# Performance work log

Measured on AMD Instinct MI355X. Metric: run time of the kernel, lower is better.

## Reference

```python
import jax, jax.numpy as jnp
import numpy as np

N_NODES = 100000
N_EDGES = 1600000
IN_FEATS = 128
N_HIDDEN = 64
N_HEADS = 4
N_CLASSES = 16


def setup_inputs() -> dict:
    key = jax.random.key(0)
    ks = jax.random.split(key, 16)
    h = jax.random.normal(ks[0], (N_NODES, IN_FEATS), dtype=jnp.float32)
    src = jax.random.randint(ks[1], (N_EDGES,), 0, N_NODES, dtype=jnp.int32)
    dst = jax.random.randint(ks[2], (N_EDGES,), 0, N_NODES, dtype=jnp.int32)
    def xavier(k, shape, fan_in, fan_out):
        gain = jnp.sqrt(2.0)  # calculate_gain('relu')
        std = gain * jnp.sqrt(2.0 / (fan_in + fan_out))
        return (std * jax.random.normal(k, shape)).astype(jnp.float32)
    # layer 1: per-head W [H, in, out], A [H, 2*out]
    W1 = xavier(ks[3], (N_HEADS, IN_FEATS, N_HIDDEN), IN_FEATS, N_HIDDEN)
    b1 = jnp.zeros((N_HEADS, N_HIDDEN), jnp.float32)
    a1 = xavier(ks[4], (N_HEADS, 2 * N_HIDDEN), 2 * N_HIDDEN, 1)
    ab1 = jnp.zeros((N_HEADS,), jnp.float32)
    # layer 2: input is concat of heads = N_HEADS*N_HIDDEN, output n_classes, heads averaged
    d2 = N_HEADS * N_HIDDEN
    W2 = xavier(ks[5], (N_HEADS, d2, N_CLASSES), d2, N_CLASSES)
    b2 = jnp.zeros((N_HEADS, N_CLASSES), jnp.float32)
    a2 = xavier(ks[6], (N_HEADS, 2 * N_CLASSES), 2 * N_CLASSES, 1)
    ab2 = jnp.zeros((N_HEADS,), jnp.float32)
    fc_w = xavier(ks[7], (N_CLASSES, N_CLASSES), N_CLASSES, N_CLASSES)
    fc_b = jnp.zeros((N_CLASSES,), jnp.float32)
    return dict(h=h, src=src, dst=dst, W1=W1, b1=b1, a1=a1, ab1=ab1,
                W2=W2, b2=b2, a2=a2, ab2=ab2, fc_w=fc_w, fc_b=fc_b)


def gat_layer(h, src, dst, W, b, a, ab, n_nodes):
    # h: [N, F]; W: [H, F, O]; a: [H, 2O]
    O = W.shape[-1]
    Wh = jnp.einsum('nf,hfo->nho', h, W) + b          # [N, H, O]
    Wh_src = Wh[src]                                   # [E, H, O] (messages Wh_j)
    Wh_dst = Wh[dst]                                   # [E, H, O] (Wh_i)
    # e_ij = LeakyReLU(A([Wh_i, Wh_j]), 0.2)
    e = (jnp.einsum('eho,ho->eh', Wh_dst, a[:, :O])
         + jnp.einsum('eho,ho->eh', Wh_src, a[:, O:]) + ab)  # [E, H]
    e = jax.nn.leaky_relu(e, 0.2)
    # segment softmax over incoming edges of each dst node
    m = jax.ops.segment_max(e, dst, num_segments=n_nodes)     # [N, H] (-inf for empty)
    ex = jnp.exp(e - m[dst])
    denom = jax.ops.segment_sum(ex, dst, num_segments=n_nodes)
    alpha = ex / denom[dst]                                    # [E, H]
    # weighted neighbor aggregation (zero for zero-in-degree nodes, as DGL)
    out = jax.ops.segment_sum(alpha[:, :, None] * Wh_src, dst, num_segments=n_nodes)
    return out  # [N, H, O]


def reference(h, src, dst, W1, b1, a1, ab1, W2, b2, a2, ab2, fc_w, fc_b):
    n = h.shape[0]
    # layer 1 (heads concatenated) + ELU; dropout = identity (eval mode)
    h1 = gat_layer(h, src, dst, W1, b1, a1, ab1, n)            # [N, H, n_hidden]
    h1 = jax.nn.elu(h1.reshape(n, -1))                         # [N, H*n_hidden]
    # layer 2 (heads averaged) + softmax over features
    h2 = gat_layer(h1, src, dst, W2, b2, a2, ab2, n).mean(axis=1)  # [N, n_classes]
    h2 = jax.nn.softmax(h2, axis=1)
    # readout: mean over nodes, then fc
    hg = h2.mean(axis=0)                                        # [n_classes]
    return hg @ fc_w.T + fc_b
```

## Files before the change

kernel.cpp:

```cpp
#include <hip/hip_runtime.h>
#include <math.h>

#define N_NODES  100000
#define N_EDGES  1600000
#define IN_F     128
#define HID      64
#define HEADS    4
#define NCLS     16
#define D1       (HEADS*HID)
#define D2       (HEADS*NCLS)

#define SCAN_CHUNK 1024
#define SCAN_NB    ((N_NODES + SCAN_CHUNK - 1) / SCAN_CHUNK)
#define N_NODES_PAD (SCAN_NB * SCAN_CHUNK)
#define RB1 128
#define AGG_BLOCKS 2048
#define AGG_WAVES  (AGG_BLOCKS * 4)

typedef __attribute__((ext_vector_type(8))) short bf16x8_t;
typedef __attribute__((ext_vector_type(4))) float f32x4_t;
typedef __attribute__((ext_vector_type(2))) float f32x2_t;

__device__ __forceinline__ unsigned bf16rne(float x) {
  unsigned u = __float_as_uint(x);
  return (u + 0x7fffu + ((u >> 16) & 1u)) >> 16;
}
__device__ __forceinline__ unsigned packbf2(float lo, float hi) {
  return bf16rne(lo) | (bf16rne(hi) << 16);
}

__global__ __launch_bounds__(256)
void k_zero4(int4* __restrict__ p, int n4) {
  int i = blockIdx.x * blockDim.x + threadIdx.x;
  if (i < n4) p[i] = make_int4(0, 0, 0, 0);
}

__global__ __launch_bounds__(256)
void k_count(const int* __restrict__ dst, int* __restrict__ cursorPad,
             int* __restrict__ rank) {
  int i = blockIdx.x * blockDim.x + threadIdx.x;
  if (i < N_EDGES) {
    int d = dst[i];
    rank[i] = atomicAdd(&cursorPad[d << 4], 1);
  }
}

__global__ __launch_bounds__(256)
void k_compact(const int* __restrict__ cursorPad, int* __restrict__ counts) {
  int i = blockIdx.x * blockDim.x + threadIdx.x;
  if (i < N_NODES_PAD) counts[i] = (i < N_NODES) ? cursorPad[i << 4] : 0;
}

__global__ __launch_bounds__(256)
void k_scanA(const int* __restrict__ counts, int* __restrict__ btot) {
  __shared__ int red[256];
  int t = threadIdx.x;
  const int4* cp = (const int4*)(counts + blockIdx.x * SCAN_CHUNK);
  int4 v = cp[t];
  red[t] = v.x + v.y + v.z + v.w;
  __syncthreads();
  for (int s = 128; s; s >>= 1) {
    if (t < s) red[t] += red[t + s];
    __syncthreads();
  }
  if (t == 0) btot[blockIdx.x] = red[0];
}

__global__ __launch_bounds__(128)
void k_scanB(const int* __restrict__ btot, int* __restrict__ bbase,
             int* __restrict__ offs) {
  __shared__ int part[128];
  int t = threadIdx.x;
  part[t] = (t < SCAN_NB) ? btot[t] : 0;
  __syncthreads();
  for (int o = 1; o < 128; o <<= 1) {
    int v = (t >= o) ? part[t - o] : 0;
    __syncthreads();
    part[t] += v;
    __syncthreads();
  }
  if (t < SCAN_NB) bbase[t] = (t == 0) ? 0 : part[t - 1];
  if (t == 0) offs[N_NODES] = N_EDGES;
}

__global__ __launch_bounds__(256)
void k_scanC(const int* __restrict__ counts, const int* __restrict__ bbase,
             int* __restrict__ offs) {
  __shared__ int part[256];
  int t = threadIdx.x;
  int gbase = blockIdx.x * SCAN_CHUNK;
  const int4* cp = (const int4*)(counts + gbase);
  int4 v = cp[t];
  int tot = v.x + v.y + v.z + v.w;
  part[t] = tot;
  __syncthreads();
  for (int o = 1; o < 256; o <<= 1) {
    int q = (t >= o) ? part[t - o] : 0;
    __syncthreads();
    part[t] += q;
    __syncthreads();
  }
  int run = bbase[blockIdx.x] + part[t] - tot;
  int i0 = gbase + t * 4;
  int o0 = run;
  int o1 = o0 + v.x;
  int o2 = o1 + v.y;
  int o3 = o2 + v.z;
  if (i0 + 0 < N_NODES) offs[i0 + 0] = o0;
  if (i0 + 1 < N_NODES) offs[i0 + 1] = o1;
  if (i0 + 2 < N_NODES) offs[i0 + 2] = o2;
  if (i0 + 3 < N_NODES) offs[i0 + 3] = o3;
}

__global__ __launch_bounds__(256)
void k_scatter(const int* __restrict__ src, const int* __restrict__ dst,
               const int* __restrict__ rank, const int* __restrict__ offs,
               int* __restrict__ csrsrc) {
  int i = blockIdx.x * blockDim.x + threadIdx.x;
  if (i < N_EDGES) {
    csrsrc[offs[dst[i]] + rank[i]] = src[i];
  }
}

__global__ __launch_bounds__(256)
void k_prepw(const float* __restrict__ W1, const float* __restrict__ W2,
             unsigned* __restrict__ W1t32, unsigned* __restrict__ W2t32) {
  int t = threadIdx.x;
  if (blockIdx.x == 0) {
    int c = t;
    const float* wp = W1 + ((c >> 6) << 13) + (c & 63);
    unsigned* op = W1t32 + c * 64;
    for (int fp = 0; fp < 64; ++fp) {
      float lo = wp[(2 * fp) << 6];
      float hi = wp[(2 * fp + 1) << 6];
      op[fp] = packbf2(lo, hi);
    }
  } else {
    int c = t & 63, fq = t >> 6;
    const float* wp = W2 + ((c >> 4) << 12) + (c & 15);
    unsigned* op = W2t32 + c * 128 + fq * 32;
    for (int fp = 0; fp < 32; ++fp) {
      int f0 = fq * 64 + 2 * fp;
      op[fp] = packbf2(wp[f0 << 4], wp[(f0 + 1) << 4]);
    }
  }
}

__global__ __launch_bounds__(256)
void k_gemm1(const float* __restrict__ h, const unsigned short* __restrict__ W1t,
             const float* __restrict__ bias, const float* __restrict__ a1,
             unsigned char* __restrict__ Wh8,
             float* __restrict__ sD, float* __restrict__ sS) {
  __shared__ float aLds[512];
  int t = threadIdx.x;
  aLds[t] = a1[t];
  aLds[t + 256] = a1[t + 256];
  __syncthreads();

  int wv = t >> 6;
  int lane = t & 63;
  int m = lane & 15;
  int q8 = (lane >> 4) * 8;
  int node = blockIdx.x * 64 + wv * 16 + m;
  int nclamp = node < N_NODES ? node : N_NODES - 1;

  f32x4_t acc[16] = {};
  const float* hp0 = h + (size_t)nclamp * IN_F + q8;
  #pragma unroll
  for (int ks = 0; ks < 4; ++ks) {
    int kk = ks * 32;
    float4 f0 = *(const float4*)(hp0 + kk);
    float4 f1 = *(const float4*)(hp0 + kk + 4);
    bf16x8_t bf;
    bf[0] = (short)bf16rne(f0.x); bf[1] = (short)bf16rne(f0.y);
    bf[2] = (short)bf16rne(f0.z); bf[3] = (short)bf16rne(f0.w);
    bf[4] = (short)bf16rne(f1.x); bf[5] = (short)bf16rne(f1.y);
    bf[6] = (short)bf16rne(f1.z); bf[7] = (short)bf16rne(f1.w);
    #pragma unroll
    for (int ct = 0; ct < 16; ++ct) {
      bf16x8_t af = *(const bf16x8_t*)(W1t + (ct * 16 + m) * IN_F + kk + q8);
      acc[ct] = __builtin_amdgcn_mfma_f32_16x16x32_bf16(af, bf, acc[ct], 0, 0, 0);
    }
  }
  if (node < N_NODES) {
    unsigned char* op = Wh8 + (size_t)node * D1;
    int quad4 = (lane >> 4) * 4;
    float pd[4] = {}, ps[4] = {};
    #pragma unroll
    for (int ct = 0; ct < 16; ++ct) {
      int c0 = ct * 16 + quad4;
      float4 bb = *(const float4*)(bias + c0);
      float v0 = acc[ct][0] + bb.x, v1 = acc[ct][1] + bb.y;
      float v2 = acc[ct][2] + bb.z, v3 = acc[ct][3] + bb.w;
      int hh = ct >> 2;
      const float* aD = &aLds[hh * 128 + (c0 & 63)];
      pd[hh] += v0 * aD[0] + v1 * aD[1] + v2 * aD[2] + v3 * aD[3];
      ps[hh] += v0 * aD[64] + v1 * aD[65] + v2 * aD[66] + v3 * aD[67];
      int pk = __builtin_amdgcn_cvt_pk_fp8_f32(v0, v1, 0, false);
      pk = __builtin_amdgcn_cvt_pk_fp8_f32(v2, v3, pk, true);
      *(unsigned*)(op + c0) = (unsigned)pk;
    }
    #pragma unroll
    for (int hh = 0; hh < 4; ++hh) {
      pd[hh] += __shfl_xor(pd[hh], 16); pd[hh] += __shfl_xor(pd[hh], 32);
      ps[hh] += __shfl_xor(ps[hh], 16); ps[hh] += __shfl_xor(ps[hh], 32);
    }
    if (lane < 16) {
      ((float4*)sD)[node] = make_float4(pd[0], pd[1], pd[2], pd[3]);
      ((float4*)sS)[node] = make_float4(ps[0], ps[1], ps[2], ps[3]);
    }
  }
}

__global__ __launch_bounds__(256)
void k_gemm2(const unsigned short* __restrict__ h1b, const unsigned short* __restrict__ W2t,
             const float* __restrict__ bias, const float* __restrict__ a2,
             unsigned short* __restrict__ Whb2,
             float* __restrict__ sD, float* __restrict__ sS) {
  __shared__ float aLds[128];
  int t = threadIdx.x;
  if (t < 128) aLds[t] = a2[t];
  __syncthreads();

  int wv = t >> 6;
  int lane = t & 63;
  int m = lane & 15;
  int q8 = (lane >> 4) * 8;
  int node = blockIdx.x * 64 + wv * 16 + m;
  int nclamp = node < N_NODES ? node : N_NODES - 1;

  f32x4_t acc[4] = {};
  const unsigned short* hp0 = h1b + (size_t)nclamp * D1 + q8;
  #pragma unroll
  for (int ks = 0; ks < 8; ++ks) {
    int kk = ks * 32;
    bf16x8_t bf = *(const bf16x8_t*)(hp0 + kk);
    #pragma unroll
    for (int ct = 0; ct < 4; ++ct) {
      bf16x8_t af = *(const bf16x8_t*)(W2t + (ct * 16 + m) * D1 + kk + q8);
      acc[ct] = __builtin_amdgcn_mfma_f32_16x16x32_bf16(af, bf, acc[ct], 0, 0, 0);
    }
  }
  if (node < N_NODES) {
    unsigned short* op = Whb2 + (size_t)node * D2;
    int quad4 = (lane >> 4) * 4;
    float pd[4] = {}, ps[4] = {};
    #pragma unroll
    for (int ct = 0; ct < 4; ++ct) {
      int c0 = ct * 16 + quad4;
      float4 bb = *(const float4*)(bias + c0);
      float v0 = acc[ct][0] + bb.x, v1 = acc[ct][1] + bb.y;
      float v2 = acc[ct][2] + bb.z, v3 = acc[ct][3] + bb.w;
      const float* aD = &aLds[ct * 32 + (c0 & 15)];
      pd[ct] += v0 * aD[0] + v1 * aD[1] + v2 * aD[2] + v3 * aD[3];
      ps[ct] += v0 * aD[16] + v1 * aD[17] + v2 * aD[18] + v3 * aD[19];
      uint2 o;
      o.x = packbf2(v0, v1);
      o.y = packbf2(v2, v3);
      *(uint2*)(op + c0) = o;
    }
    #pragma unroll
    for (int hh = 0; hh < 4; ++hh) {
      pd[hh] += __shfl_xor(pd[hh], 16); pd[hh] += __shfl_xor(pd[hh], 32);
      ps[hh] += __shfl_xor(ps[hh], 16); ps[hh] += __shfl_xor(ps[hh], 32);
    }
    if (lane < 16) {
      ((float4*)sD)[node] = make_float4(pd[0], pd[1], pd[2], pd[3]);
      ((float4*)sS)[node] = make_float4(ps[0], ps[1], ps[2], ps[3]);
    }
  }
}

__device__ __forceinline__ float lrelu(float x) { return x > 0.f ? x : 0.2f * x; }
__device__ __forceinline__ float elu(float x)   { return x > 0.f ? x : expm1f(x); }

__global__ __launch_bounds__(256)
void k_agg1(const int* __restrict__ offs, const int* __restrict__ csrsrc,
            const float* __restrict__ sD, const float* __restrict__ sS,
            const float* __restrict__ ab,
            const unsigned char* __restrict__ Wh8, unsigned short* __restrict__ h1out) {
  __shared__ float exbuf[4][64 * 4];
  __shared__ int   offbuf[4][64];
  int wv = threadIdx.x >> 6;
  int lane = threadIdx.x & 63;
  int g = lane >> 5;
  int l = lane & 31;
  int hh = l >> 3;
  unsigned lb = (unsigned)(l << 3);
  float ab0 = ab[0], ab1 = ab[1], ab2 = ab[2], ab3 = ab[3];
  const float* eb = exbuf[wv];
  const int* ob = offbuf[wv];

  for (int wid = blockIdx.x * 4 + wv; wid < N_NODES; wid += AGG_WAVES) {
    float acc[8] = {};
    float z0 = 0.f, z1 = 0.f, z2 = 0.f, z3 = 0.f;
    int beg = offs[wid], end = offs[wid + 1];
    bool nonempty = end > beg;
    if (nonempty) {
      float4 dv = ((const float4*)sD)[wid];
      float db0 = dv.x + ab0, db1 = dv.y + ab1;
      float db2 = dv.z + ab2, db3 = dv.w + ab3;
      for (int cbeg = beg; cbeg < end; cbeg += 64) {
        int j = cbeg + lane;
        int cnt = end - cbeg; if (cnt > 64) cnt = 64;
        int sid = 0;
        float e0 = 0.f, e1 = 0.f, e2 = 0.f, e3 = 0.f;
        if (j < end) {
          sid = csrsrc[j];
          float4 sv = ((const float4*)sS)[sid];
          e0 = __expf(lrelu(db0 + sv.x));
          e1 = __expf(lrelu(db1 + sv.y));
          e2 = __expf(lrelu(db2 + sv.z));
          e3 = __expf(lrelu(db3 + sv.w));
          z0 += e0; z1 += e1; z2 += e2; z3 += e3;
        }
        offbuf[wv][lane] = sid << 8;
        *(float4*)&exbuf[wv][lane * 4] = make_float4(e0, e1, e2, e3);
        int npairs = (cnt + 1) >> 1;
        int nh = (npairs + 1) >> 1;
        for (int u = 0; u < nh; ++u) {
          int iA = 2 * u + g;
          int iB = iA + 2 * nh;
          float wA = eb[iA * 4 + hh];
          float wB = eb[iB * 4 + hh];
          unsigned vA = (unsigned)ob[iA] + lb;
          unsigned vB = (unsigned)ob[iB] + lb;
          uint2 pA = *(const uint2*)(Wh8 + vA);
          uint2 pB = *(const uint2*)(Wh8 + vB);
          f32x2_t a0 = __builtin_amdgcn_cvt_pk_f32_fp8(pA.x, false);
          f32x2_t a1v = __builtin_amdgcn_cvt_pk_f32_fp8(pA.x, true);
          f32x2_t a2v = __builtin_amdgcn_cvt_pk_f32_fp8(pA.y, false);
          f32x2_t a3 = __builtin_amdgcn_cvt_pk_f32_fp8(pA.y, true);
          acc[0] = fmaf(wA, a0[0], acc[0]);
          acc[1] = fmaf(wA, a0[1], acc[1]);
          acc[2] = fmaf(wA, a1v[0], acc[2]);
          acc[3] = fmaf(wA, a1v[1], acc[3]);
          acc[4] = fmaf(wA, a2v[0], acc[4]);
          acc[5] = fmaf(wA, a2v[1], acc[5]);
          acc[6] = fmaf(wA, a3[0], acc[6]);
          acc[7] = fmaf(wA, a3[1], acc[7]);
          f32x2_t b0 = __builtin_amdgcn_cvt_pk_f32_fp8(pB.x, false);
          f32x2_t b1 = __builtin_amdgcn_cvt_pk_f32_fp8(pB.x, true);
          f32x2_t b2 = __builtin_amdgcn_cvt_pk_f32_fp8(pB.y, false);
          f32x2_t b3 = __builtin_amdgcn_cvt_pk_f32_fp8(pB.y, true);
          acc[0] = fmaf(wB, b0[0], acc[0]);
          acc[1] = fmaf(wB, b0[1], acc[1]);
          acc[2] = fmaf(wB, b1[0], acc[2]);
          acc[3] = fmaf(wB, b1[1], acc[3]);
          acc[4] = fmaf(wB, b2[0], acc[4]);
          acc[5] = fmaf(wB, b2[1], acc[5]);
          acc[6] = fmaf(wB, b3[0], acc[6]);
          acc[7] = fmaf(wB, b3[1], acc[7]);
        }
      }
      #pragma unroll
      for (int o = 32; o; o >>= 1) {
        z0 += __shfl_xor(z0, o);
        z1 += __shfl_xor(z1, o);
        z2 += __shfl_xor(z2, o);
        z3 += __shfl_xor(z3, o);
      }
    }
    #pragma unroll
    for (int i = 0; i < 8; ++i) acc[i] += __shfl_xor(acc[i], 32);
    float z = (hh == 0) ? z0 : (hh == 1) ? z1 : (hh == 2) ? z2 : z3;
    if (!nonempty) z = 1.f;
    float inv = 1.f / z;
    if (g == 0) {
      float e0 = elu(acc[0] * inv), e1 = elu(acc[1] * inv);
      float e2 = elu(acc[2] * inv), e3 = elu(acc[3] * inv);
      float e4 = elu(acc[4] * inv), e5 = elu(acc[5] * inv);
      float e6 = elu(acc[6] * inv), e7 = elu(acc[7] * inv);
      uint4 o;
      o.x = packbf2(e0, e1);
      o.y = packbf2(e2, e3);
      o.z = packbf2(e4, e5);
      o.w = packbf2(e6, e7);
      *(uint4*)(h1out + (size_t)wid * D1 + l * 8) = o;
    }
  }
}

__global__ __launch_bounds__(256)
void k_agg2(const int* __restrict__ offs, const int* __restrict__ csrsrc,
            const float* __restrict__ sD, const float* __restrict__ sS,
            const float* __restrict__ ab,
            const unsigned short* __restrict__ Whb2, float* __restrict__ partials) {
  __shared__ float exbuf[4][64 * 4];
  __shared__ int   offbuf[4][64];
  __shared__ float red[4][16];
  int wv = threadIdx.x >> 6;
  int lane = threadIdx.x & 63;
  int g = lane >> 4;
  int l = lane & 15;
  int hh = l >> 2;
  unsigned lb = (unsigned)(l << 3);
  float ab0 = ab[0], ab1 = ab[1], ab2 = ab[2], ab3 = ab[3];
  const float* eb = exbuf[wv];
  const int* ob = offbuf[wv];
  float smacc[4] = {};

  for (int wid = blockIdx.x * 4 + wv; wid < N_NODES; wid += AGG_WAVES) {
    float acc[4] = {};
    float z0 = 0.f, z1 = 0.f, z2 = 0.f, z3 = 0.f;
    int beg = offs[wid], end = offs[wid + 1];
    bool nonempty = end > beg;
    if (nonempty) {
      float4 dv = ((const float4*)sD)[wid];
      float db0 = dv.x + ab0, db1 = dv.y + ab1;
      float db2 = dv.z + ab2, db3 = dv.w + ab3;
      for (int cbeg = beg; cbeg < end; cbeg += 64) {
        int j = cbeg + lane;
        int cnt = end - cbeg; if (cnt > 64) cnt = 64;
        int sid = 0;
        float e0 = 0.f, e1 = 0.f, e2 = 0.f, e3 = 0.f;
        if (j < end) {
          sid = csrsrc[j];
          float4 sv = ((const float4*)sS)[sid];
          e0 = __expf(lrelu(db0 + sv.x));
          e1 = __expf(lrelu(db1 + sv.y));
          e2 = __expf(lrelu(db2 + sv.z));
          e3 = __expf(lrelu(db3 + sv.w));
          z0 += e0; z1 += e1; z2 += e2; z3 += e3;
        }
        offbuf[wv][lane] = sid << 7;
        *(float4*)&exbuf[wv][lane * 4] = make_float4(e0, e1, e2, e3);
        int ni = (cnt + 3) >> 2;
        int nh2 = (ni + 1) >> 1;
        for (int it = 0; it < nh2; ++it) {
          int qA = 4 * it + g;
          int qB = qA + 4 * nh2;
          float wA = eb[qA * 4 + hh];
          float wB = eb[qB * 4 + hh];
          unsigned vA = (unsigned)ob[qA] + lb;
          unsigned vB = (unsigned)ob[qB] + lb;
          uint2 pA = *(const uint2*)((const unsigned char*)Whb2 + vA);
          uint2 pB = *(const uint2*)((const unsigned char*)Whb2 + vB);
          acc[0] = fmaf(wA, __uint_as_float(pA.x << 16), acc[0]);
          acc[1] = fmaf(wA, __uint_as_float(pA.x & 0xffff0000u), acc[1]);
          acc[2] = fmaf(wA, __uint_as_float(pA.y << 16), acc[2]);
          acc[3] = fmaf(wA, __uint_as_float(pA.y & 0xffff0000u), acc[3]);
          acc[0] = fmaf(wB, __uint_as_float(pB.x << 16), acc[0]);
          acc[1] = fmaf(wB, __uint_as_float(pB.x & 0xffff0000u), acc[1]);
          acc[2] = fmaf(wB, __uint_as_float(pB.y << 16), acc[2]);
          acc[3] = fmaf(wB, __uint_as_float(pB.y & 0xffff0000u), acc[3]);
        }
      }
      #pragma unroll
      for (int s = 32; s; s >>= 1) {
        z0 += __shfl_xor(z0, s);
        z1 += __shfl_xor(z1, s);
        z2 += __shfl_xor(z2, s);
        z3 += __shfl_xor(z3, s);
      }
    }
    #pragma unroll
    for (int i = 0; i < 4; ++i) {
      acc[i] += __shfl_xor(acc[i], 16);
      acc[i] += __shfl_xor(acc[i], 32);
    }
    float z = (hh == 0) ? z0 : (hh == 1) ? z1 : (hh == 2) ? z2 : z3;
    if (!nonempty) z = 1.f;
    float inv = 1.f / z;
    float val[4];
    #pragma unroll
    for (int i = 0; i < 4; ++i) val[i] = acc[i] * inv;
    #pragma unroll
    for (int i = 0; i < 4; ++i) {
      val[i] += __shfl_xor(val[i], 4);
      val[i] += __shfl_xor(val[i], 8);
      val[i] *= 0.25f;
    }
    float mx = fmaxf(fmaxf(val[0], val[1]), fmaxf(val[2], val[3]));
    mx = fmaxf(mx, __shfl_xor(mx, 1));
    mx = fmaxf(mx, __shfl_xor(mx, 2));
    float e[4];
    float ssum = 0.f;
    #pragma unroll
    for (int i = 0; i < 4; ++i) { e[i] = __expf(val[i] - mx); ssum += e[i]; }
    ssum += __shfl_xor(ssum, 1);
    ssum += __shfl_xor(ssum, 2);
    float rinv = 1.f / ssum;
    #pragma unroll
    for (int i = 0; i < 4; ++i) smacc[i] += e[i] * rinv;
  }

  if (g == 0 && l < 4) {
    #pragma unroll
    for (int i = 0; i < 4; ++i) red[wv][l * 4 + i] = smacc[i];
  }
  __syncthreads();
  if (threadIdx.x < 16) {
    partials[(size_t)blockIdx.x * 16 + threadIdx.x] =
        red[0][threadIdx.x] + red[1][threadIdx.x] +
        red[2][threadIdx.x] + red[3][threadIdx.x];
  }
}

__global__ __launch_bounds__(256)
void k_reduce1(const float* __restrict__ partials, int nrows,
               float* __restrict__ out) {
  __shared__ float red[16][17];
  int t = threadIdx.x;
  int c = t & 15, rl = t >> 4;
  int per = (nrows + RB1 - 1) / RB1;
  int rbeg = blockIdx.x * per;
  int rend = rbeg + per; if (rend > nrows) rend = nrows;
  float s = 0.f;
  for (int r = rbeg + rl; r < rend; r += 16) s += partials[(size_t)r * 16 + c];
  red[rl][c] = s;
  __syncthreads();
  for (int st = 8; st; st >>= 1) {
    if (rl < st) red[rl][c] += red[rl + st][c];
    __syncthreads();
  }
  if (t < 16) out[(size_t)blockIdx.x * 16 + t] = red[0][t];
}

__global__ __launch_bounds__(256)
void k_final(const float* __restrict__ partials,
             const float* __restrict__ fcw, const float* __restrict__ fcb,
             float* __restrict__ out) {
  __shared__ float red[16][17];
  __shared__ float hg[16];
  int t = threadIdx.x;
  int c = t & 15, rl = t >> 4;
  float s = 0.f;
  for (int r = rl; r < RB1; r += 16) s += partials[(size_t)r * 16 + c];
  red[rl][c] = s;
  __syncthreads();
  for (int st = 8; st; st >>= 1) {
    if (rl < st) red[rl][c] += red[rl + st][c];
    __syncthreads();
  }
  if (t < 16) hg[t] = red[0][t] * (1.0f / N_NODES);
  __syncthreads();
  if (t < 16) {
    float acc = fcb[t];
    #pragma unroll
    for (int k = 0; k < 16; ++k) acc += hg[k] * fcw[t * 16 + k];
    out[t] = acc;
  }
}

extern "C" void kernel_launch(void* const* d_in, const int* in_sizes, int n_in,
                              void* d_out, int out_size, void* d_ws, size_t ws_size,
                              hipStream_t stream) {
  const float* h   = (const float*)d_in[0];
  const int*   src = (const int*)  d_in[1];
  const int*   dst = (const int*)  d_in[2];
  const float* W1  = (const float*)d_in[3];
  const float* b1  = (const float*)d_in[4];
  const float* a1  = (const float*)d_in[5];
  const float* ab1 = (const float*)d_in[6];
  const float* W2  = (const float*)d_in[7];
  const float* b2  = (const float*)d_in[8];
  const float* a2  = (const float*)d_in[9];
  const float* ab2 = (const float*)d_in[10];
  const float* fcw = (const float*)d_in[11];
  const float* fcb = (const float*)d_in[12];
  float* out = (float*)d_out;

  char* ws = (char*)d_ws;
  size_t off = 0;
  auto alloc = [&](size_t bytes) -> char* {
    char* p = ws + off;
    off += (bytes + 255) & ~(size_t)255;
    return p;
  };
  unsigned char*  Wh8  = (unsigned char*)alloc((size_t)N_NODES * D1);
  unsigned short* h1b  = (unsigned short*)alloc((size_t)N_NODES * D1 * 2);
  unsigned short* Whb2 = (unsigned short*)alloc((size_t)N_NODES * D2 * 2);
  unsigned short* W1t  = (unsigned short*)alloc((size_t)D1 * IN_F * 2);
  unsigned short* W2t  = (unsigned short*)alloc((size_t)D2 * D1 * 2);
  float* sD1 = (float*)alloc((size_t)N_NODES * 4 * 4);
  float* sS1 = (float*)alloc((size_t)N_NODES * 4 * 4);
  float* sD2 = (float*)alloc((size_t)N_NODES * 4 * 4);
  float* sS2 = (float*)alloc((size_t)N_NODES * 4 * 4);
  int* cursorPad = (int*)alloc((size_t)N_NODES * 16 * 4);
  int* rank   = (int*)alloc((size_t)N_EDGES * 4);
  int* counts = (int*)alloc((size_t)N_NODES_PAD * 4);
  int* offs   = (int*)alloc((size_t)(N_NODES + 1) * 4);
  int* csrsrc = (int*)alloc((size_t)N_EDGES * 4);
  int* btot   = (int*)alloc((size_t)SCAN_NB * 4);
  int* bbase  = (int*)alloc((size_t)SCAN_NB * 4);
  float* partials  = (float*)alloc((size_t)AGG_BLOCKS * 16 * 4);
  float* partials2 = (float*)alloc((size_t)RB1 * 16 * 4);

  k_prepw<<<2, 256, 0, stream>>>(W1, W2, (unsigned*)W1t, (unsigned*)W2t);

  const int n4 = N_NODES * 4;
  k_zero4<<<(n4 + 255) / 256, 256, 0, stream>>>((int4*)cursorPad, n4);
  k_count<<<(N_EDGES + 255) / 256, 256, 0, stream>>>(dst, cursorPad, rank);
  k_compact<<<(N_NODES_PAD + 255) / 256, 256, 0, stream>>>(cursorPad, counts);
  k_scanA<<<SCAN_NB, 256, 0, stream>>>(counts, btot);
  k_scanB<<<1, 128, 0, stream>>>(btot, bbase, offs);
  k_scanC<<<SCAN_NB, 256, 0, stream>>>(counts, bbase, offs);
  k_scatter<<<(N_EDGES + 255) / 256, 256, 0, stream>>>(src, dst, rank, offs, csrsrc);

  const int gemmBlocks = (N_NODES + 63) / 64;

  k_gemm1<<<gemmBlocks, 256, 0, stream>>>(h, W1t, b1, a1, Wh8, sD1, sS1);
  k_agg1<<<AGG_BLOCKS, 256, 0, stream>>>(offs, csrsrc, sD1, sS1, ab1, Wh8, h1b);

  k_gemm2<<<gemmBlocks, 256, 0, stream>>>(h1b, W2t, b2, a2, Whb2, sD2, sS2);
  k_agg2<<<AGG_BLOCKS, 256, 0, stream>>>(offs, csrsrc, sD2, sS2, ab2, Whb2, partials);

  k_reduce1<<<RB1, 256, 0, stream>>>(partials, AGG_BLOCKS, partials2);
  k_final<<<1, 256, 0, stream>>>(partials2, fcw, fcb, out);
}
```

Measured before the change: 480.6 us.

## Fuse CSR-build kernels, vectorize edge passes, use packed FMA in aggregation

Merges weight prep with the cursor zeroing, and the count compaction with the first scan stage. This removes two launches. The edge count and scatter kernels now process four edges per thread with int4 loads. The gemm1 launch moves between count and scan. Both aggregation kernels switch to packed two-wide f32 FMA on vector accumulators to cut VALU instruction count. Risks are extra register shuffling for the vector splits and unchanged atomic contention.

```diff
diff --git a/kernel.cpp b/kernel.cpp
--- a/kernel.cpp
+++ b/kernel.cpp
@@ -16,6 +16,9 @@
 #define RB1 128
 #define AGG_BLOCKS 2048
 #define AGG_WAVES  (AGG_BLOCKS * 4)
+#define GEMM1_BLOCKS ((N_NODES + 63) / 64)
+#define EDGE4_BLOCKS ((N_EDGES / 4 + 255) / 256)
+#define ZERO_BLOCKS  ((N_NODES * 4 + 255) / 256)
 
 typedef __attribute__((ext_vector_type(8))) short bf16x8_t;
 typedef __attribute__((ext_vector_type(4))) float f32x4_t;
@@ -28,36 +31,65 @@
 __device__ __forceinline__ unsigned packbf2(float lo, float hi) {
   return bf16rne(lo) | (bf16rne(hi) << 16);
 }
-
-__global__ __launch_bounds__(256)
-void k_zero4(int4* __restrict__ p, int n4) {
-  int i = blockIdx.x * blockDim.x + threadIdx.x;
-  if (i < n4) p[i] = make_int4(0, 0, 0, 0);
-}
-
-__global__ __launch_bounds__(256)
-void k_count(const int* __restrict__ dst, int* __restrict__ cursorPad,
-             int* __restrict__ rank) {
-  int i = blockIdx.x * blockDim.x + threadIdx.x;
-  if (i < N_EDGES) {
-    int d = dst[i];
-    rank[i] = atomicAdd(&cursorPad[d << 4], 1);
-  }
-}
-
-__global__ __launch_bounds__(256)
-void k_compact(const int* __restrict__ cursorPad, int* __restrict__ counts) {
-  int i = blockIdx.x * blockDim.x + threadIdx.x;
-  if (i < N_NODES_PAD) counts[i] = (i < N_NODES) ? cursorPad[i << 4] : 0;
-}
-
-__global__ __launch_bounds__(256)
-void k_scanA(const int* __restrict__ counts, int* __restrict__ btot) {
+__device__ __forceinline__ f32x2_t pkfma(f32x2_t a, f32x2_t b, f32x2_t c) {
+  return __builtin_elementwise_fma(a, b, c);
+}
+
+__global__ __launch_bounds__(256)
+void k_prep(const float* __restrict__ W1, const float* __restrict__ W2,
+            unsigned* __restrict__ W1t32, unsigned* __restrict__ W2t32,
+            int4* __restrict__ cursorPad4) {
+  int t = threadIdx.x;
+  if (blockIdx.x == 0) {
+    int c = t;
+    const float* wp = W1 + ((c >> 6) << 13) + (c & 63);
+    unsigned* op = W1t32 + c * 64;
+    for (int fp = 0; fp < 64; ++fp) {
+      float lo = wp[(2 * fp) << 6];
+      float hi = wp[(2 * fp + 1) << 6];
+      op[fp] = packbf2(lo, hi);
+    }
+  } else if (blockIdx.x == 1) {
+    int c = t & 63, fq = t >> 6;
+    const float* wp = W2 + ((c >> 4) << 12) + (c & 15);
+    unsigned* op = W2t32 + c * 128 + fq * 32;
+    for (int fp = 0; fp < 32; ++fp) {
+      int f0 = fq * 64 + 2 * fp;
+      op[fp] = packbf2(wp[f0 << 4], wp[(f0 + 1) << 4]);
+    }
+  } else {
+    int i = (blockIdx.x - 2) * 256 + t;
+    if (i < N_NODES * 4) cursorPad4[i] = make_int4(0, 0, 0, 0);
+  }
+}
+
+__global__ __launch_bounds__(256)
+void k_count4(const int* __restrict__ dst, int* __restrict__ cursorPad,
+              int* __restrict__ rank) {
+  int v = blockIdx.x * blockDim.x + threadIdx.x;
+  if (v < N_EDGES / 4) {
+    int4 d = ((const int4*)dst)[v];
+    int r0 = atomicAdd(&cursorPad[d.x << 4], 1);
+    int r1 = atomicAdd(&cursorPad[d.y << 4], 1);
+    int r2 = atomicAdd(&cursorPad[d.z << 4], 1);
+    int r3 = atomicAdd(&cursorPad[d.w << 4], 1);
+    ((int4*)rank)[v] = make_int4(r0, r1, r2, r3);
+  }
+}
+
+__global__ __launch_bounds__(256)
+void k_scanAc(const int* __restrict__ cursorPad, int* __restrict__ counts,
+              int* __restrict__ btot) {
   __shared__ int red[256];
   int t = threadIdx.x;
-  const int4* cp = (const int4*)(counts + blockIdx.x * SCAN_CHUNK);
-  int4 v = cp[t];
-  red[t] = v.x + v.y + v.z + v.w;
+  int gbase = blockIdx.x * SCAN_CHUNK;
+  int i0 = gbase + t * 4;
+  int c0 = (i0 + 0 < N_NODES) ? cursorPad[(i0 + 0) << 4] : 0;
+  int c1 = (i0 + 1 < N_NODES) ? cursorPad[(i0 + 1) << 4] : 0;
+  int c2 = (i0 + 2 < N_NODES) ? cursorPad[(i0 + 2) << 4] : 0;
+  int c3 = (i0 + 3 < N_NODES) ? cursorPad[(i0 + 3) << 4] : 0;
+  ((int4*)counts)[(gbase >> 2) + t] = make_int4(c0, c1, c2, c3);
+  red[t] = c0 + c1 + c2 + c3;
   __syncthreads();
   for (int s = 128; s; s >>= 1) {
     if (t < s) red[t] += red[t + s];
@@ -113,36 +145,19 @@
 }
 
 __global__ __launch_bounds__(256)
-void k_scatter(const int* __restrict__ src, const int* __restrict__ dst,
-               const int* __restrict__ rank, const int* __restrict__ offs,
-               int* __restrict__ csrsrc) {
-  int i = blockIdx.x * blockDim.x + threadIdx.x;
-  if (i < N_EDGES) {
-    csrsrc[offs[dst[i]] + rank[i]] = src[i];
-  }
-}
-
-__global__ __launch_bounds__(256)
-void k_prepw(const float* __restrict__ W1, const float* __restrict__ W2,
-             unsigned* __restrict__ W1t32, unsigned* __restrict__ W2t32) {
-  int t = threadIdx.x;
-  if (blockIdx.x == 0) {
-    int c = t;
-    const float* wp = W1 + ((c >> 6) << 13) + (c & 63);
-    unsigned* op = W1t32 + c * 64;
-    for (int fp = 0; fp < 64; ++fp) {
-      float lo = wp[(2 * fp) << 6];
-      float hi = wp[(2 * fp + 1) << 6];
-      op[fp] = packbf2(lo, hi);
-    }
-  } else {
-    int c = t & 63, fq = t >> 6;
-    const float* wp = W2 + ((c >> 4) << 12) + (c & 15);
-    unsigned* op = W2t32 + c * 128 + fq * 32;
-    for (int fp = 0; fp < 32; ++fp) {
-      int f0 = fq * 64 + 2 * fp;
-      op[fp] = packbf2(wp[f0 << 4], wp[(f0 + 1) << 4]);
-    }
+void k_scatter4(const int* __restrict__ src, const int* __restrict__ dst,
+                const int* __restrict__ rank, const int* __restrict__ offs,
+                int* __restrict__ csrsrc) {
+  int v = blockIdx.x * blockDim.x + threadIdx.x;
+  if (v < N_EDGES / 4) {
+    int4 d = ((const int4*)dst)[v];
+    int4 r = ((const int4*)rank)[v];
+    int4 s = ((const int4*)src)[v];
+    int o0 = offs[d.x], o1 = offs[d.y], o2 = offs[d.z], o3 = offs[d.w];
+    csrsrc[o0 + r.x] = s.x;
+    csrsrc[o1 + r.y] = s.y;
+    csrsrc[o2 + r.z] = s.z;
+    csrsrc[o3 + r.w] = s.w;
   }
 }
 
@@ -292,7 +307,7 @@
   const int* ob = offbuf[wv];
 
   for (int wid = blockIdx.x * 4 + wv; wid < N_NODES; wid += AGG_WAVES) {
-    float acc[8] = {};
+    f32x2_t acc[4] = {};
     float z0 = 0.f, z1 = 0.f, z2 = 0.f, z3 = 0.f;
     int beg = offs[wid], end = offs[wid + 1];
     bool nonempty = end > beg;
@@ -327,30 +342,16 @@
           unsigned vB = (unsigned)ob[iB] + lb;
           uint2 pA = *(const uint2*)(Wh8 + vA);
           uint2 pB = *(const uint2*)(Wh8 + vB);
-          f32x2_t a0 = __builtin_amdgcn_cvt_pk_f32_fp8(pA.x, false);
-          f32x2_t a1v = __builtin_amdgcn_cvt_pk_f32_fp8(pA.x, true);
-          f32x2_t a2v = __builtin_amdgcn_cvt_pk_f32_fp8(pA.y, false);
-          f32x2_t a3 = __builtin_amdgcn_cvt_pk_f32_fp8(pA.y, true);
-          acc[0] = fmaf(wA, a0[0], acc[0]);
-          acc[1] = fmaf(wA, a0[1], acc[1]);
-          acc[2] = fmaf(wA, a1v[0], acc[2]);
-          acc[3] = fmaf(wA, a1v[1], acc[3]);
-          acc[4] = fmaf(wA, a2v[0], acc[4]);
-          acc[5] = fmaf(wA, a2v[1], acc[5]);
-          acc[6] = fmaf(wA, a3[0], acc[6]);
-          acc[7] = fmaf(wA, a3[1], acc[7]);
-          f32x2_t b0 = __builtin_amdgcn_cvt_pk_f32_fp8(pB.x, false);
-          f32x2_t b1 = __builtin_amdgcn_cvt_pk_f32_fp8(pB.x, true);
-          f32x2_t b2 = __builtin_amdgcn_cvt_pk_f32_fp8(pB.y, false);
-          f32x2_t b3 = __builtin_amdgcn_cvt_pk_f32_fp8(pB.y, true);
-          acc[0] = fmaf(wB, b0[0], acc[0]);
-          acc[1] = fmaf(wB, b0[1], acc[1]);
-          acc[2] = fmaf(wB, b1[0], acc[2]);
-          acc[3] = fmaf(wB, b1[1], acc[3]);
-          acc[4] = fmaf(wB, b2[0], acc[4]);
-          acc[5] = fmaf(wB, b2[1], acc[5]);
-          acc[6] = fmaf(wB, b3[0], acc[6]);
-          acc[7] = fmaf(wB, b3[1], acc[7]);
+          f32x2_t wa2 = {wA, wA};
+          acc[0] = pkfma(wa2, __builtin_amdgcn_cvt_pk_f32_fp8(pA.x, false), acc[0]);
+          acc[1] = pkfma(wa2, __builtin_amdgcn_cvt_pk_f32_fp8(pA.x, true ), acc[1]);
+          acc[2] = pkfma(wa2, __builtin_amdgcn_cvt_pk_f32_fp8(pA.y, false), acc[2]);
+          acc[3] = pkfma(wa2, __builtin_amdgcn_cvt_pk_f32_fp8(pA.y, true ), acc[3]);
+          f32x2_t wb2 = {wB, wB};
+          acc[0] = pkfma(wb2, __builtin_amdgcn_cvt_pk_f32_fp8(pB.x, false), acc[0]);
+          acc[1] = pkfma(wb2, __builtin_amdgcn_cvt_pk_f32_fp8(pB.x, true ), acc[1]);
+          acc[2] = pkfma(wb2, __builtin_amdgcn_cvt_pk_f32_fp8(pB.y, false), acc[2]);
+          acc[3] = pkfma(wb2, __builtin_amdgcn_cvt_pk_f32_fp8(pB.y, true ), acc[3]);
         }
       }
       #pragma unroll
@@ -362,20 +363,19 @@
       }
     }
     #pragma unroll
-    for (int i = 0; i < 8; ++i) acc[i] += __shfl_xor(acc[i], 32);
+    for (int i = 0; i < 4; ++i) {
+      acc[i][0] += __shfl_xor(acc[i][0], 32);
+      acc[i][1] += __shfl_xor(acc[i][1], 32);
+    }
     float z = (hh == 0) ? z0 : (hh == 1) ? z1 : (hh == 2) ? z2 : z3;
     if (!nonempty) z = 1.f;
     float inv = 1.f / z;
     if (g == 0) {
-      float e0 = elu(acc[0] * inv), e1 = elu(acc[1] * inv);
-      float e2 = elu(acc[2] * inv), e3 = elu(acc[3] * inv);
-      float e4 = elu(acc[4] * inv), e5 = elu(acc[5] * inv);
-      float e6 = elu(acc[6] * inv), e7 = elu(acc[7] * inv);
       uint4 o;
-      o.x = packbf2(e0, e1);
-      o.y = packbf2(e2, e3);
-      o.z = packbf2(e4, e5);
-      o.w = packbf2(e6, e7);
+      o.x = packbf2(elu(acc[0][0] * inv), elu(acc[0][1] * inv));
+      o.y = packbf2(elu(acc[1][0] * inv), elu(acc[1][1] * inv));
+      o.z = packbf2(elu(acc[2][0] * inv), elu(acc[2][1] * inv));
+      o.w = packbf2(elu(acc[3][0] * inv), elu(acc[3][1] * inv));
       *(uint4*)(h1out + (size_t)wid * D1 + l * 8) = o;
     }
   }
@@ -401,7 +401,7 @@
   float smacc[4] = {};
 
   for (int wid = blockIdx.x * 4 + wv; wid < N_NODES; wid += AGG_WAVES) {
-    float acc[4] = {};
+    f32x2_t acc[2] = {};
     float z0 = 0.f, z1 = 0.f, z2 = 0.f, z3 = 0.f;
     int beg = offs[wid], end = offs[wid + 1];
     bool nonempty = end > beg;
@@ -436,14 +436,18 @@
           unsigned vB = (unsigned)ob[qB] + lb;
           uint2 pA = *(const uint2*)((const unsigned char*)Whb2 + vA);
           uint2 pB = *(const uint2*)((const unsigned char*)Whb2 + vB);
-          acc[0] = fmaf(wA, __uint_as_float(pA.x << 16), acc[0]);
-          acc[1] = fmaf(wA, __uint_as_float(pA.x & 0xffff0000u), acc[1]);
-          acc[2] = fmaf(wA, __uint_as_float(pA.y << 16), acc[2]);
-          acc[3] = fmaf(wA, __uint_as_float(pA.y & 0xffff0000u), acc[3]);
-          acc[0] = fmaf(wB, __uint_as_float(pB.x << 16), acc[0]);
-          acc[1] = fmaf(wB, __uint_as_float(pB.x & 0xffff0000u), acc[1]);
-          acc[2] = fmaf(wB, __uint_as_float(pB.y << 16), acc[2]);
-          acc[3] = fmaf(wB, __uint_as_float(pB.y & 0xffff0000u), acc[3]);
+          f32x2_t wa2 = {wA, wA};
+          f32x2_t dA0, dA1;
+          dA0[0] = __uint_as_float(pA.x << 16); dA0[1] = __uint_as_float(pA.x & 0xffff0000u);
+          dA1[0] = __uint_as_float(pA.y << 16); dA1[1] = __uint_as_float(pA.y & 0xffff0000u);
+          acc[0] = pkfma(wa2, dA0, acc[0]);
+          acc[1] = pkfma(wa2, dA1, acc[1]);
+          f32x2_t wb2 = {wB, wB};
+          f32x2_t dB0, dB1;
+          dB0[0] = __uint_as_float(pB.x << 16); dB0[1] = __uint_as_float(pB.x & 0xffff0000u);
+          dB1[0] = __uint_as_float(pB.y << 16); dB1[1] = __uint_as_float(pB.y & 0xffff0000u);
+          acc[0] = pkfma(wb2, dB0, acc[0]);
+          acc[1] = pkfma(wb2, dB1, acc[1]);
         }
       }
       #pragma unroll
@@ -455,16 +459,20 @@
       }
     }
     #pragma unroll
-    for (int i = 0; i < 4; ++i) {
-      acc[i] += __shfl_xor(acc[i], 16);
-      acc[i] += __shfl_xor(acc[i], 32);
+    for (int i = 0; i < 2; ++i) {
+      acc[i][0] += __shfl_xor(acc[i][0], 16);
+      acc[i][1] += __shfl_xor(acc[i][1], 16);
+      acc[i][0] += __shfl_xor(acc[i][0], 32);
+      acc[i][1] += __shfl_xor(acc[i][1], 32);
     }
     float z = (hh == 0) ? z0 : (hh == 1) ? z1 : (hh == 2) ? z2 : z3;
     if (!nonempty) z = 1.f;
     float inv = 1.f / z;
     float val[4];
-    #pragma unroll
-    for (int i = 0; i < 4; ++i) val[i] = acc[i] * inv;
+    val[0] = acc[0][0] * inv;
+    val[1] = acc[0][1] * inv;
+    val[2] = acc[1][0] * inv;
+    val[3] = acc[1][1] * inv;
     #pragma unroll
     for (int i = 0; i < 4; ++i) {
       val[i] += __shfl_xor(val[i], 4);
@@ -587,23 +595,21 @@
   float* partials  = (float*)alloc((size_t)AGG_BLOCKS * 16 * 4);
   float* partials2 = (float*)alloc((size_t)RB1 * 16 * 4);
 
-  k_prepw<<<2, 256, 0, stream>>>(W1, W2, (unsigned*)W1t, (unsigned*)W2t);
-
-  const int n4 = N_NODES * 4;
-  k_zero4<<<(n4 + 255) / 256, 256, 0, stream>>>((int4*)cursorPad, n4);
-  k_count<<<(N_EDGES + 255) / 256, 256, 0, stream>>>(dst, cursorPad, rank);
-  k_compact<<<(N_NODES_PAD + 255) / 256, 256, 0, stream>>>(cursorPad, counts);
-  k_scanA<<<SCAN_NB, 256, 0, stream>>>(counts, btot);
+  k_prep<<<2 + ZERO_BLOCKS, 256, 0, stream>>>(W1, W2, (unsigned*)W1t, (unsigned*)W2t,
+                                              (int4*)cursorPad);
+
+  k_count4<<<EDGE4_BLOCKS, 256, 0, stream>>>(dst, cursorPad, rank);
+
+  k_gemm1<<<GEMM1_BLOCKS, 256, 0, stream>>>(h, W1t, b1, a1, Wh8, sD1, sS1);
+
+  k_scanAc<<<SCAN_NB, 256, 0, stream>>>(cursorPad, counts, btot);
   k_scanB<<<1, 128, 0, stream>>>(btot, bbase, offs);
   k_scanC<<<SCAN_NB, 256, 0, stream>>>(counts, bbase, offs);
-  k_scatter<<<(N_EDGES + 255) / 256, 256, 0, stream>>>(src, dst, rank, offs, csrsrc);
-
-  const int gemmBlocks = (N_NODES + 63) / 64;
-
-  k_gemm1<<<gemmBlocks, 256, 0, stream>>>(h, W1t, b1, a1, Wh8, sD1, sS1);
+  k_scatter4<<<EDGE4_BLOCKS, 256, 0, stream>>>(src, dst, rank, offs, csrsrc);
+
   k_agg1<<<AGG_BLOCKS, 256, 0, stream>>>(offs, csrsrc, sD1, sS1, ab1, Wh8, h1b);
 
-  k_gemm2<<<gemmBlocks, 256, 0, stream>>>(h1b, W2t, b2, a2, Whb2, sD2, sS2);
+  k_gemm2<<<GEMM1_BLOCKS, 256, 0, stream>>>(h1b, W2t, b2, a2, Whb2, sD2, sS2);
   k_agg2<<<AGG_BLOCKS, 256, 0, stream>>>(offs, csrsrc, sD2, sS2, ab2, Whb2, partials);
 
   k_reduce1<<<RB1, 256, 0, stream>>>(partials, AGG_BLOCKS, partials2);
```

Result: no change. 480.7 us (+0.0%).
